# Kernel tuning notes

Measured on AMD Instinct MI355X. Metric: run time of the kernel, lower is better.

The kernel has to match this reference:

```python
import jax, jax.numpy as jnp
import numpy as np


def setup_inputs() -> dict:
    key = jax.random.key(0)
    k1, k2, k3, k4 = jax.random.split(key, 4)
    B, S, D_IN, D_OUT = 4, 2048, 4096, 16384
    inp = jax.random.normal(k1, (B, S, D_IN), dtype=jnp.float32)
    # int8-valued quantized weight stored as int32 (values in [-127, 127])
    quant_w = jax.random.randint(k2, (D_OUT, D_IN), -127, 128, dtype=jnp.int32)
    # per-output-channel scale (weight.abs().max / 127 in the original); keep positive
    scale_w = jax.random.uniform(k3, (D_OUT,), dtype=jnp.float32, minval=0.005, maxval=0.02)
    bias = jax.random.normal(k4, (D_OUT,), dtype=jnp.float32)
    return {"inp": inp, "quant_w": quant_w, "scale_w": scale_w, "bias": bias}


def reference(inp, quant_w, scale_w, bias):
    # extract_weight_to_half (bit_width=8): w_fp = int8_weight * scale[:, None]
    weight = quant_w.astype(scale_w.dtype) * scale_w[:, None]  # [D_OUT, D_IN]
    # W8A16Linear.forward: flatten tokens, mm with weight.T, add bias
    out = jnp.einsum('bsd,od->bso', inp, weight)  # [B, S, D_OUT]
    return out + bias
```

## Files before the change

### kernel.cpp

```cpp
#include <hip/hip_runtime.h>
#include <stdint.h>

typedef __attribute__((ext_vector_type(4))) int iv4;
typedef __attribute__((ext_vector_type(16))) char i8x16;

#define BM 256
#define BN 256
#define BKB 128

__global__ __launch_bounds__(256) void quant_act(const float* __restrict__ in,
                                                 signed char* __restrict__ out,
                                                 float* __restrict__ s_a,
                                                 int K) {
  const int row = blockIdx.x;
  const int t = threadIdx.x;
  const float* a = in + (long)row * K;
  float4 v[4];
#pragma unroll
  for (int i = 0; i < 4; ++i)
    v[i] = reinterpret_cast<const float4*>(a)[t * 4 + i];
  float m = 0.f;
#pragma unroll
  for (int i = 0; i < 4; ++i) {
    m = fmaxf(m, fmaxf(fmaxf(fabsf(v[i].x), fabsf(v[i].y)),
                       fmaxf(fabsf(v[i].z), fabsf(v[i].w))));
  }
#pragma unroll
  for (int off = 32; off; off >>= 1) m = fmaxf(m, __shfl_xor(m, off));
  __shared__ float wmax[4];
  const int lane = t & 63, wvq = t >> 6;
  if (lane == 0) wmax[wvq] = m;
  __syncthreads();
  m = fmaxf(fmaxf(wmax[0], wmax[1]), fmaxf(wmax[2], wmax[3]));
  const float inv = m > 0.f ? 127.f / m : 0.f;
  if (t == 0) s_a[row] = m > 0.f ? m / 127.f : 0.f;
  i8x16 q;
#pragma unroll
  for (int i = 0; i < 4; ++i) {
    q[i * 4 + 0] = (char)(int)rintf(fminf(fmaxf(v[i].x * inv, -127.f), 127.f));
    q[i * 4 + 1] = (char)(int)rintf(fminf(fmaxf(v[i].y * inv, -127.f), 127.f));
    q[i * 4 + 2] = (char)(int)rintf(fminf(fmaxf(v[i].z * inv, -127.f), 127.f));
    q[i * 4 + 3] = (char)(int)rintf(fminf(fmaxf(v[i].w * inv, -127.f), 127.f));
  }
  reinterpret_cast<i8x16*>(out + (long)row * K)[t] = q;
}

__global__ void pack_w(const int* __restrict__ in, signed char* __restrict__ out,
                       long n16) {
  long stride = (long)gridDim.x * blockDim.x;
  for (long i = (long)blockIdx.x * blockDim.x + threadIdx.x; i < n16; i += stride) {
    i8x16 q;
#pragma unroll
    for (int c = 0; c < 4; ++c) {
      int4 w = reinterpret_cast<const int4*>(in)[i * 4 + c];
      q[c * 4 + 0] = (char)w.x;
      q[c * 4 + 1] = (char)w.y;
      q[c * 4 + 2] = (char)w.z;
      q[c * 4 + 3] = (char)w.w;
    }
    reinterpret_cast<i8x16*>(out)[i] = q;
  }
}

#define GLDS16(g, l)                                                          \
  __builtin_amdgcn_global_load_lds(                                           \
      (const __attribute__((address_space(1))) unsigned int*)(g),             \
      (__attribute__((address_space(3))) unsigned int*)(l), 16, 0, 0)

typedef __attribute__((address_space(3))) const signed char lds_c8;

template <int OFF>
__device__ __forceinline__ iv4 ldsb128(lds_c8* p) {
  iv4 r;
  asm volatile("ds_read_b128 %0, %1 offset:%2" : "=v"(r) : "v"(p), "i"(OFF));
  return r;
}

#define BAR __builtin_amdgcn_s_barrier()
#define SCHEDB __builtin_amdgcn_sched_barrier(0)
#define LGKM_0 asm volatile("s_waitcnt lgkmcnt(0)")
#define LGKM_8 asm volatile("s_waitcnt lgkmcnt(8)")
#define VMC_4 asm volatile("s_waitcnt vmcnt(4)")

#define PH_MFMA(AF, BQ, I0, J0)                                               \
  _Pragma("unroll") for (int i = 0; i < 4; ++i)                               \
    _Pragma("unroll") for (int jj = 0; jj < 2; ++jj)                          \
      _Pragma("unroll") for (int ks = 0; ks < 2; ++ks)                        \
        acc[(I0) + i][(J0) + jj] = __builtin_amdgcn_mfma_i32_16x16x64_i8(     \
            AF[i][ks], BQ[jj][ks], acc[(I0) + i][(J0) + jj], 0, 0, 0)

__global__ __launch_bounds__(512, 2) void gemm256_m2(
    const signed char* __restrict__ A,
    const signed char* __restrict__ W,
    const float* __restrict__ s_a,
    const float* __restrict__ scale,
    const float* __restrict__ bias,
    float* __restrict__ C,
    int M, int N, int K) {
  __shared__ __align__(16) signed char As[2][2][128 * 128];
  __shared__ __align__(16) signed char Bs[2][2][128 * 128];

  const int tid = threadIdx.x;
  const int lane = tid & 63;
  const int wv = tid >> 6;
  const int wm = wv >> 2;
  const int wn = wv & 3;

  const int nwg = gridDim.x;
  const int bid = blockIdx.x;
  const int wg = ((nwg & 7) == 0) ? ((bid & 7) * (nwg >> 3) + (bid >> 3)) : bid;
  const int mT = M / BM;
  const int bm = wg % mT;
  const int bn = wg / mT;

  const long aRow0 = (long)bm * BM;
  const long wRow0 = (long)bn * BN;

  const int sRow0 = (0 * 8 + wv) * 8 + (lane >> 3);
  const int sRow1 = (1 * 8 + wv) * 8 + (lane >> 3);
  const int srcslot = (lane & 7) ^ (((wv & 1) << 2) | (lane >> 4));
  const signed char* aS0 = A + (aRow0 + sRow0) * (long)K + srcslot * 16;
  const signed char* aS1 = A + (aRow0 + sRow1) * (long)K + srcslot * 16;
  const signed char* wS0 = W + (wRow0 + sRow0) * (long)K + srcslot * 16;
  const signed char* wS1 = W + (wRow0 + sRow1) * (long)K + srcslot * 16;
  const long AH = 128 * (long)K;
  const int d0 = (0 * 8 + wv) * 1024 + lane * 16;
  const int d1 = (1 * 8 + wv) * 1024 + lane * 16;

  const int rdLane = (lane & 15) * 128 + (((lane >> 4) ^ ((lane >> 1) & 7)) * 16);
  const int rdB_off = (wn & 1) * 8192;

  iv4 acc[8][4] = {};
  iv4 aF[4][2], bQ0[2][2], bQ1[2][2];

  const int nk = K / BKB;

  GLDS16(aS0, &As[0][0][d0]);           GLDS16(aS1, &As[0][0][d1]);
  GLDS16(aS0 + AH, &As[0][1][d0]);      GLDS16(aS1 + AH, &As[0][1][d1]);
  GLDS16(wS0, &Bs[0][0][d0]);           GLDS16(wS1, &Bs[0][0][d1]);
  GLDS16(wS0 + AH, &Bs[0][1][d0]);      GLDS16(wS1 + AH, &Bs[0][1][d1]);
  GLDS16(wS0 + AH + BKB, &Bs[1][1][d0]); GLDS16(wS1 + AH + BKB, &Bs[1][1][d1]);
  GLDS16(aS0 + BKB, &As[1][0][d0]);     GLDS16(aS1 + BKB, &As[1][0][d1]);
  VMC_4;
  BAR;

#define TILE_BODY(CUR, NXT, KO1, KO2)                                         \
  {                                                                           \
    lds_c8* pAk0 = (lds_c8*)&As[CUR][wm][rdLane];                             \
    lds_c8* pAk1 = (lds_c8*)&As[CUR][wm][rdLane ^ 64];                        \
    lds_c8* pBk0 = (lds_c8*)&Bs[CUR][wn >> 1][rdB_off + rdLane];              \
    lds_c8* pBk1 = (lds_c8*)&Bs[CUR][wn >> 1][rdB_off + (rdLane ^ 64)];       \
                                    \
    bQ0[0][0] = ldsb128<0>(pBk0);    bQ0[0][1] = ldsb128<0>(pBk1);            \
    bQ0[1][0] = ldsb128<2048>(pBk0); bQ0[1][1] = ldsb128<2048>(pBk1);         \
    aF[0][0] = ldsb128<0>(pAk0);     aF[0][1] = ldsb128<0>(pAk1);             \
    aF[1][0] = ldsb128<2048>(pAk0);  aF[1][1] = ldsb128<2048>(pAk1);          \
    aF[2][0] = ldsb128<4096>(pAk0);  aF[2][1] = ldsb128<4096>(pAk1);          \
    aF[3][0] = ldsb128<6144>(pAk0);  aF[3][1] = ldsb128<6144>(pAk1);          \
    GLDS16(aS0 + AH + (KO1), &As[NXT][1][d0]);                                \
    GLDS16(aS1 + AH + (KO1), &As[NXT][1][d1]);                                \
    LGKM_8; SCHEDB;                                                           \
    BAR;                                                                      \
    LGKM_0; SCHEDB;                                                           \
    __builtin_amdgcn_s_setprio(1);                                            \
    PH_MFMA(aF, bQ0, 0, 0);                                                   \
    __builtin_amdgcn_s_setprio(0);                                            \
    SCHEDB; BAR;                                                              \
                                     \
    bQ1[0][0] = ldsb128<4096>(pBk0); bQ1[0][1] = ldsb128<4096>(pBk1);         \
    bQ1[1][0] = ldsb128<6144>(pBk0); bQ1[1][1] = ldsb128<6144>(pBk1);         \
    GLDS16(wS0 + (KO1), &Bs[NXT][0][d0]);                                     \
    GLDS16(wS1 + (KO1), &Bs[NXT][0][d1]);                                     \
    BAR;                                                                      \
    LGKM_0; SCHEDB;                                                           \
    __builtin_amdgcn_s_setprio(1);                                            \
    PH_MFMA(aF, bQ1, 0, 2);                                                   \
    __builtin_amdgcn_s_setprio(0);                                            \
    SCHEDB; BAR;                                                              \
                                     \
    aF[0][0] = ldsb128<8192>(pAk0);  aF[0][1] = ldsb128<8192>(pAk1);          \
    aF[1][0] = ldsb128<10240>(pAk0); aF[1][1] = ldsb128<10240>(pAk1);         \
    aF[2][0] = ldsb128<12288>(pAk0); aF[2][1] = ldsb128<12288>(pAk1);         \
    aF[3][0] = ldsb128<14336>(pAk0); aF[3][1] = ldsb128<14336>(pAk1);         \
    GLDS16(wS0 + AH + (KO2), &Bs[CUR][1][d0]);                                \
    GLDS16(wS1 + AH + (KO2), &Bs[CUR][1][d1]);                                \
    BAR;                                                                      \
    LGKM_0; SCHEDB;                                                           \
    __builtin_amdgcn_s_setprio(1);                                            \
    PH_MFMA(aF, bQ1, 4, 2);                                                   \
    __builtin_amdgcn_s_setprio(0);                                            \
    SCHEDB; BAR;                                                              \
      \
    GLDS16(aS0 + (KO2), &As[CUR][0][d0]);                                     \
    GLDS16(aS1 + (KO2), &As[CUR][0][d1]);                                     \
    __builtin_amdgcn_s_setprio(1);                                            \
    PH_MFMA(aF, bQ0, 4, 0);                                                   \
    __builtin_amdgcn_s_setprio(0);                                            \
    VMC_4; SCHEDB;                                                            \
    BAR;                                                                      \
  }

  for (int kt = 0; kt < nk; kt += 2) {
    const long ka1 = (long)(kt + 1) * BKB;
    const long ka2 = (kt + 2 < nk) ? (long)(kt + 2) * BKB : 0;
    const long kb1 = ka2;
    const long kb2 = (kt + 3 < nk) ? (long)(kt + 3) * BKB : 0;
    TILE_BODY(0, 1, ka1, ka2);
    TILE_BODY(1, 0, kb1, kb2);
  }
#undef TILE_BODY

  const long col0 = wRow0 + wn * 64 + (lane & 15);
  float scl[4], bs[4];
#pragma unroll
  for (int j = 0; j < 4; ++j) {
    scl[j] = scale[col0 + j * 16];
    bs[j] = bias[col0 + j * 16];
  }
  const long row0 = aRow0 + wm * 128 + ((lane >> 4) << 2);
#pragma unroll
  for (int i = 0; i < 8; ++i) {
#pragma unroll
    for (int v = 0; v < 4; ++v) {
      const float rs = s_a[row0 + i * 16 + v];
      float* cp = C + (row0 + i * 16 + v) * (long)N + col0;
#pragma unroll
      for (int j = 0; j < 4; ++j)
        cp[j * 16] = (float)acc[i][j][v] * (rs * scl[j]) + bs[j];
    }
  }
}

__global__ void naive_w8a16(const float* __restrict__ inp,
                            const int* __restrict__ qw,
                            const float* __restrict__ scale,
                            const float* __restrict__ bias,
                            float* __restrict__ out, long M, long N, long K) {
  long idx = (long)blockIdx.x * blockDim.x + threadIdx.x;
  if (idx >= M * N) return;
  long col = idx % N, row = idx / N;
  const float* a = inp + row * K;
  const int* w = qw + col * K;
  float s = 0.f;
  for (long k = 0; k < K; k += 4) {
    float4 av = *reinterpret_cast<const float4*>(&a[k]);
    int4 wv = *reinterpret_cast<const int4*>(&w[k]);
    s += av.x * (float)wv.x + av.y * (float)wv.y + av.z * (float)wv.z +
         av.w * (float)wv.w;
  }
  out[idx] = s * scale[col] + bias[col];
}

extern "C" void kernel_launch(void* const* d_in, const int* in_sizes, int n_in,
                              void* d_out, int out_size, void* d_ws,
                              size_t ws_size, hipStream_t stream) {
  const float* inp = (const float*)d_in[0];
  const int* qw = (const int*)d_in[1];
  const float* scale = (const float*)d_in[2];
  const float* bias = (const float*)d_in[3];
  float* out = (float*)d_out;

  const long N = in_sizes[2];
  const long K = (long)in_sizes[1] / N;
  const long M = (long)in_sizes[0] / K;

  const size_t aB = (size_t)M * K;
  const size_t wB = (size_t)N * K;
  const size_t sB = (size_t)M * 4;
  const long nk = K / BKB;

  if (ws_size >= aB + wB + sB && (M % BM) == 0 && (N % BN) == 0 &&
      K == 4096 && nk >= 4 && (nk % 2) == 0) {
    signed char* Ai8 = (signed char*)d_ws;
    signed char* Wi8 = (signed char*)d_ws + aB;
    float* sA = (float*)((char*)d_ws + aB + wB);
    quant_act<<<(int)M, 256, 0, stream>>>(inp, Ai8, sA, (int)K);
    pack_w<<<2048, 256, 0, stream>>>(qw, Wi8, N * K / 16);
    const int nwg = (int)((M / BM) * (N / BN));
    gemm256_m2<<<nwg, 512, 0, stream>>>(Ai8, Wi8, sA, scale, bias, out,
                                        (int)M, (int)N, (int)K);
  } else {
    long total = M * N;
    naive_w8a16<<<(int)((total + 255) / 256), 256, 0, stream>>>(
        inp, qw, scale, bias, out, M, N, K);
  }
}
```

Before: 694.0 us.

## Switch int8 GEMM from 16x16x64 to 32x32x32 MFMA tiles

Result: slower. 722.4 us (+4.1%).

```diff
diff --git a/kernel.cpp b/kernel.cpp
--- a/kernel.cpp
+++ b/kernel.cpp
@@ -2,6 +2,7 @@
 #include <stdint.h>
 
 typedef __attribute__((ext_vector_type(4))) int iv4;
+typedef __attribute__((ext_vector_type(16))) int iv16;
 typedef __attribute__((ext_vector_type(16))) char i8x16;
 
 #define BM 256
@@ -82,14 +83,13 @@
 #define LGKM_8 asm volatile("s_waitcnt lgkmcnt(8)")
 #define VMC_4 asm volatile("s_waitcnt vmcnt(4)")
 
-#define PH_MFMA(AF, BQ, I0, J0)                                               \
-  _Pragma("unroll") for (int i = 0; i < 4; ++i)                               \
-    _Pragma("unroll") for (int jj = 0; jj < 2; ++jj)                          \
-      _Pragma("unroll") for (int ks = 0; ks < 2; ++ks)                        \
-        acc[(I0) + i][(J0) + jj] = __builtin_amdgcn_mfma_i32_16x16x64_i8(     \
-            AF[i][ks], BQ[jj][ks], acc[(I0) + i][(J0) + jj], 0, 0, 0)
-
-__global__ __launch_bounds__(512, 2) void gemm256_m2(
+#define PH8(AA, BB, TI0, TJ)                                                  \
+  _Pragma("unroll") for (int ks = 0; ks < 4; ++ks)                            \
+    _Pragma("unroll") for (int t = 0; t < 2; ++t)                             \
+      acc[(TI0) + t][TJ] = __builtin_amdgcn_mfma_i32_32x32x32_i8(             \
+          AA[t][ks], BB[ks], acc[(TI0) + t][TJ], 0, 0, 0)
+
+__global__ __launch_bounds__(512, 2) void gemm256_m3(
     const signed char* __restrict__ A,
     const signed char* __restrict__ W,
     const float* __restrict__ s_a,
@@ -127,11 +127,14 @@
   const int d0 = (0 * 8 + wv) * 1024 + lane * 16;
   const int d1 = (1 * 8 + wv) * 1024 + lane * 16;
 
-  const int rdLane = (lane & 15) * 128 + (((lane >> 4) ^ ((lane >> 1) & 7)) * 16);
-  const int rdB_off = (wn & 1) * 8192;
-
-  iv4 acc[8][4] = {};
-  iv4 aF[4][2], bQ0[2][2], bQ1[2][2];
+  const int rd32 = (lane & 31) * 128 + (((lane >> 5) ^ ((lane >> 1) & 7)) * 16);
+  int rdx[4];
+#pragma unroll
+  for (int ks = 0; ks < 4; ++ks) rdx[ks] = rd32 ^ (ks * 32);
+  const int rdBo = (wn & 1) * 8192;
+
+  iv16 acc[4][2] = {};
+  iv4 aF[2][4], bQ0[4], bQ1[4];
 
   const int nk = K / BKB;
 
@@ -146,55 +149,57 @@
 
 #define TILE_BODY(CUR, NXT, KO1, KO2)                                         \
   {                                                                           \
-    lds_c8* pAk0 = (lds_c8*)&As[CUR][wm][rdLane];                             \
-    lds_c8* pAk1 = (lds_c8*)&As[CUR][wm][rdLane ^ 64];                        \
-    lds_c8* pBk0 = (lds_c8*)&Bs[CUR][wn >> 1][rdB_off + rdLane];              \
-    lds_c8* pBk1 = (lds_c8*)&Bs[CUR][wn >> 1][rdB_off + (rdLane ^ 64)];       \
-                                    \
-    bQ0[0][0] = ldsb128<0>(pBk0);    bQ0[0][1] = ldsb128<0>(pBk1);            \
-    bQ0[1][0] = ldsb128<2048>(pBk0); bQ0[1][1] = ldsb128<2048>(pBk1);         \
-    aF[0][0] = ldsb128<0>(pAk0);     aF[0][1] = ldsb128<0>(pAk1);             \
-    aF[1][0] = ldsb128<2048>(pAk0);  aF[1][1] = ldsb128<2048>(pAk1);          \
-    aF[2][0] = ldsb128<4096>(pAk0);  aF[2][1] = ldsb128<4096>(pAk1);          \
-    aF[3][0] = ldsb128<6144>(pAk0);  aF[3][1] = ldsb128<6144>(pAk1);          \
+    lds_c8* pA[4];                                                            \
+    lds_c8* pB[4];                                                            \
+    _Pragma("unroll") for (int ks = 0; ks < 4; ++ks) {                        \
+      pA[ks] = (lds_c8*)&As[CUR][wm][rdx[ks]];                                \
+      pB[ks] = (lds_c8*)&Bs[CUR][wn >> 1][rdBo + rdx[ks]];                    \
+    }                                                                         \
+                     \
+    bQ0[0] = ldsb128<0>(pB[0]); bQ0[1] = ldsb128<0>(pB[1]);                   \
+    bQ0[2] = ldsb128<0>(pB[2]); bQ0[3] = ldsb128<0>(pB[3]);                   \
+    aF[0][0] = ldsb128<0>(pA[0]);    aF[1][0] = ldsb128<4096>(pA[0]);         \
+    aF[0][1] = ldsb128<0>(pA[1]);    aF[1][1] = ldsb128<4096>(pA[1]);         \
+    aF[0][2] = ldsb128<0>(pA[2]);    aF[1][2] = ldsb128<4096>(pA[2]);         \
+    aF[0][3] = ldsb128<0>(pA[3]);    aF[1][3] = ldsb128<4096>(pA[3]);         \
     GLDS16(aS0 + AH + (KO1), &As[NXT][1][d0]);                                \
     GLDS16(aS1 + AH + (KO1), &As[NXT][1][d1]);                                \
     LGKM_8; SCHEDB;                                                           \
     BAR;                                                                      \
     LGKM_0; SCHEDB;                                                           \
     __builtin_amdgcn_s_setprio(1);                                            \
-    PH_MFMA(aF, bQ0, 0, 0);                                                   \
+    PH8(aF, bQ0, 0, 0);                                                       \
     __builtin_amdgcn_s_setprio(0);                                            \
     SCHEDB; BAR;                                                              \
-                                     \
-    bQ1[0][0] = ldsb128<4096>(pBk0); bQ1[0][1] = ldsb128<4096>(pBk1);         \
-    bQ1[1][0] = ldsb128<6144>(pBk0); bQ1[1][1] = ldsb128<6144>(pBk1);         \
+                     \
+    bQ1[0] = ldsb128<4096>(pB[0]); bQ1[1] = ldsb128<4096>(pB[1]);             \
+    bQ1[2] = ldsb128<4096>(pB[2]); bQ1[3] = ldsb128<4096>(pB[3]);             \
     GLDS16(wS0 + (KO1), &Bs[NXT][0][d0]);                                     \
     GLDS16(wS1 + (KO1), &Bs[NXT][0][d1]);                                     \
     BAR;                                                                      \
     LGKM_0; SCHEDB;                                                           \
     __builtin_amdgcn_s_setprio(1);                                            \
-    PH_MFMA(aF, bQ1, 0, 2);                                                   \
+    PH8(aF, bQ1, 0, 1);                                                       \
     __builtin_amdgcn_s_setprio(0);                                            \
     SCHEDB; BAR;                                                              \
-                                     \
-    aF[0][0] = ldsb128<8192>(pAk0);  aF[0][1] = ldsb128<8192>(pAk1);          \
-    aF[1][0] = ldsb128<10240>(pAk0); aF[1][1] = ldsb128<10240>(pAk1);         \
-    aF[2][0] = ldsb128<12288>(pAk0); aF[2][1] = ldsb128<12288>(pAk1);         \
-    aF[3][0] = ldsb128<14336>(pAk0); aF[3][1] = ldsb128<14336>(pAk1);         \
+                   \
+    aF[0][0] = ldsb128<8192>(pA[0]); aF[1][0] = ldsb128<12288>(pA[0]);        \
+    aF[0][1] = ldsb128<8192>(pA[1]); aF[1][1] = ldsb128<12288>(pA[1]);        \
+    aF[0][2] = ldsb128<8192>(pA[2]); aF[1][2] = ldsb128<12288>(pA[2]);        \
+    aF[0][3] = ldsb128<8192>(pA[3]); aF[1][3] = ldsb128<12288>(pA[3]);        \
     GLDS16(wS0 + AH + (KO2), &Bs[CUR][1][d0]);                                \
     GLDS16(wS1 + AH + (KO2), &Bs[CUR][1][d1]);                                \
     BAR;                                                                      \
     LGKM_0; SCHEDB;                                                           \
     __builtin_amdgcn_s_setprio(1);                                            \
-    PH_MFMA(aF, bQ1, 4, 2);                                                   \
+    PH8(aF, bQ1, 2, 1);                                                       \
     __builtin_amdgcn_s_setprio(0);                                            \
     SCHEDB; BAR;                                                              \
-      \
+          \
     GLDS16(aS0 + (KO2), &As[CUR][0][d0]);                                     \
     GLDS16(aS1 + (KO2), &As[CUR][0][d1]);                                     \
     __builtin_amdgcn_s_setprio(1);                                            \
-    PH_MFMA(aF, bQ0, 4, 0);                                                   \
+    PH8(aF, bQ0, 2, 0);                                                       \
     __builtin_amdgcn_s_setprio(0);                                            \
     VMC_4; SCHEDB;                                                            \
     BAR;                                                                      \
@@ -210,23 +215,28 @@
   }
 #undef TILE_BODY
 
-  const long col0 = wRow0 + wn * 64 + (lane & 15);
-  float scl[4], bs[4];
-#pragma unroll
-  for (int j = 0; j < 4; ++j) {
-    scl[j] = scale[col0 + j * 16];
-    bs[j] = bias[col0 + j * 16];
-  }
-  const long row0 = aRow0 + wm * 128 + ((lane >> 4) << 2);
-#pragma unroll
-  for (int i = 0; i < 8; ++i) {
-#pragma unroll
-    for (int v = 0; v < 4; ++v) {
-      const float rs = s_a[row0 + i * 16 + v];
-      float* cp = C + (row0 + i * 16 + v) * (long)N + col0;
-#pragma unroll
-      for (int j = 0; j < 4; ++j)
-        cp[j * 16] = (float)acc[i][j][v] * (rs * scl[j]) + bs[j];
+  const long col0 = wRow0 + wn * 64 + (lane & 31);
+  float scl[2], bs[2];
+#pragma unroll
+  for (int tj = 0; tj < 2; ++tj) {
+    scl[tj] = scale[col0 + tj * 32];
+    bs[tj] = bias[col0 + tj * 32];
+  }
+  const long row0 = aRow0 + wm * 128 + ((lane >> 5) << 2);
+#pragma unroll
+  for (int ti = 0; ti < 4; ++ti) {
+#pragma unroll
+    for (int q = 0; q < 4; ++q) {
+      const long rbase = row0 + ti * 32 + q * 8;
+#pragma unroll
+      for (int r = 0; r < 4; ++r) {
+        const long row = rbase + r;
+        const float rs = s_a[row];
+        float* cp = C + row * (long)N + col0;
+#pragma unroll
+        for (int tj = 0; tj < 2; ++tj)
+          cp[tj * 32] = (float)acc[ti][tj][q * 4 + r] * (rs * scl[tj]) + bs[tj];
+      }
     }
   }
 }
@@ -277,7 +287,7 @@
     quant_act<<<(int)M, 256, 0, stream>>>(inp, Ai8, sA, (int)K);
     pack_w<<<2048, 256, 0, stream>>>(qw, Wi8, N * K / 16);
     const int nwg = (int)((M / BM) * (N / BN));
-    gemm256_m2<<<nwg, 512, 0, stream>>>(Ai8, Wi8, sA, scale, bias, out,
+    gemm256_m3<<<nwg, 512, 0, stream>>>(Ai8, Wi8, sA, scale, bias, out,
                                         (int)M, (int)N, (int)K);
   } else {
     long total = M * N;
```
